# Optimization experiments

Measured on AMD Instinct MI355X. Metric: run time of the kernel, lower is better.

The kernel has to match this reference:

```python
import jax, jax.numpy as jnp
import numpy as np

K_SIGN = 100000.0   # tanh sharpness approximating sign()
EPS = 1e-05         # acos clamp epsilon


def setup_inputs() -> dict:
    key = jax.random.key(0)
    B, N, KV = 2, 8, 64
    contour = jax.random.uniform(key, (B, N, KV, 2), dtype=jnp.float32)  # values in [0,1]
    return {"contour": contour, "size": 128}


def reference(contour, size):
    b, n, kv, _ = contour.shape
    dt = contour.dtype
    # pixel grid, normalized by size (matches torch meshgrid 'ij' + reshape(-1,2)/size)
    g = jnp.arange(size, dtype=dt)
    mesh = jnp.stack(jnp.meshgrid(g, g, indexing="ij"), axis=-1).reshape(-1, 2) / size  # (S2, 2)

    c = contour.reshape(b * n, 1, kv, 2)          # (bn, 1, kv, 2)
    diff = c - mesh[None, :, None, :]             # (bn, S2, kv, 2)
    roll_diff = jnp.roll(diff, -1, axis=2)        # next vertex

    # sign = diff * swap(roll_diff); sign[...,1]-sign[...,0] = d_y*rd_x - d_x*rd_y
    cross = diff[..., 1] * roll_diff[..., 0] - diff[..., 0] * roll_diff[..., 1]
    sign = jnp.tanh(K_SIGN * cross)               # (bn, S2, kv)

    norm_diff = jnp.linalg.norm(diff, axis=3)
    norm_roll = jnp.linalg.norm(roll_diff, axis=3)
    scalar = jnp.sum(diff * roll_diff, axis=3)
    cosang = jnp.clip(scalar / (norm_diff * norm_roll), -1.0 + EPS, 1.0 - EPS)
    angles = jnp.arccos(cosang)                   # (bn, S2, kv)

    sum_angles = jnp.clip(jnp.abs(jnp.sum(sign * angles, axis=2) / (2.0 * jnp.pi)), 0.0, 1.0)
    return sum_angles.reshape(b, n, size, size)
```

## Files before the change

### kernel.cpp

```cpp
#include <hip/hip_runtime.h>
#include <math.h>

#define BLOCK 256
#define SPLIT 4
#define MAX_KV_LDS 1024

__device__ __forceinline__ float fast_tanh_k(float cross)
{
    float e = __expf(cross * 200000.0f);
    return fmaf(-2.0f, __builtin_amdgcn_rcpf(e + 1.0f), 1.0f);
}

__device__ __forceinline__ float fast_acos(float x)
{
    float y = fabsf(x);
    float p = fmaf(-0.0187293f, y, 0.0742610f);
    p = fmaf(p, y, -0.2121144f);
    p = fmaf(p, y, 1.5707288f);
    float a = sqrtf(1.0f - y) * p;
    return (x >= 0.0f) ? a : (3.14159265358979f - a);
}

template <typename VP>
__device__ __forceinline__ float winding_partial(VP vsrc, int kv, int k0, int k1,
                                                 float mx, float my)
{
    float acc = 0.0f;
    if (k0 >= k1) return acc;
    float2 v = vsrc[k0];
    float dx = v.x - mx, dy = v.y - my;
    float nd2 = fmaf(dx, dx, dy * dy);

    #pragma unroll 4
    for (int k = k0; k < k1; ++k) {
        int kn = k + 1;
        if (kn == kv) kn = 0;
        float2 vn = vsrc[kn];
        float rx = vn.x - mx, ry = vn.y - my;
        float cross = dy * rx - dx * ry;
        float dot   = fmaf(dx, rx, dy * ry);
        float nr2   = fmaf(rx, rx, ry * ry);
        float cosang = dot * __builtin_amdgcn_rsqf(nd2 * nr2);
        cosang = __builtin_amdgcn_fmed3f(cosang, -1.0f + 1e-5f, 1.0f - 1e-5f);
        acc = fmaf(fast_tanh_k(cross), fast_acos(cosang), acc);
        dx = rx; dy = ry; nd2 = nr2;
    }
    return acc;
}

__global__ __launch_bounds__(BLOCK)
void contour_mask_kernel(const float2* __restrict__ contour,
                         const int* __restrict__ size_ptr,
                         float* __restrict__ out,
                         int out_size, int in0_elems)
{
    __shared__ float2 verts[MAX_KV_LDS];

    const int size     = *size_ptr;
    const int S2       = size * size;
    const int bn_total = out_size / S2;
    const int kv       = in0_elems / (bn_total * 2);

    const int tid   = threadIdx.x;
    const int idx4  = blockIdx.x * BLOCK + tid;
    const int pixel = idx4 >> 2;
    const int seg   = tid & (SPLIT - 1);

    const int p_first = (blockIdx.x * BLOCK) >> 2;
    const int p_last  = ((blockIdx.x + 1) * BLOCK - 1) >> 2;
    const int bn0     = p_first / S2;
    const bool use_lds = (kv <= MAX_KV_LDS) && (bn0 == p_last / S2);

    if (use_lds) {
        for (int i = tid; i < kv; i += BLOCK)
            verts[i] = contour[(size_t)bn0 * kv + i];
    }
    __syncthreads();

    float acc = 0.0f;
    if (pixel < out_size) {
        const int bn = pixel / S2;
        const int p  = pixel - bn * S2;
        const float inv_size = 1.0f / (float)size;
        const int pi = p / size;
        const int pj = p - pi * size;
        const float mx = (float)pi * inv_size;
        const float my = (float)pj * inv_size;

        const int q  = (kv + SPLIT - 1) / SPLIT;
        const int k0 = seg * q;
        const int k1 = min(k0 + q, kv);

        if (use_lds)
            acc = winding_partial(verts, kv, k0, k1, mx, my);
        else
            acc = winding_partial(contour + (size_t)bn * kv, kv, k0, k1, mx, my);
    }

    acc += __shfl_xor(acc, 1, 64);
    acc += __shfl_xor(acc, 2, 64);

    if (pixel < out_size && seg == 0) {
        float res = fabsf(acc) * 0.15915494309189535f;
        out[pixel] = fminf(res, 1.0f);
    }
}

extern "C" void kernel_launch(void* const* d_in, const int* in_sizes, int n_in,
                              void* d_out, int out_size, void* d_ws, size_t ws_size,
                              hipStream_t stream)
{
    const float2* contour  = (const float2*)d_in[0];
    const int*    size_ptr = (const int*)d_in[1];
    float*        out      = (float*)d_out;

    const long long threads = (long long)out_size * SPLIT;
    const int blocks = (int)((threads + BLOCK - 1) / BLOCK);
    contour_mask_kernel<<<blocks, BLOCK, 0, stream>>>(
        contour, size_ptr, out, out_size, in_sizes[0]);
}
```

Measured before the change: 77.79 us.

## Process two pixels per thread with packed float2 vector math

Each thread now evaluates two adjacent pixels against the same vertex segment, using 2-wide vector types so the compiler can emit packed FP32 ops (v_pk_fma/mul). Each vertex value loaded from LDS is reused across both pixels, and the grid shrinks by half. Results are written as float2. Transcendentals stay scalar, so the gain is limited to the arithmetic and load portions, and halving the thread count may reduce latency hiding.

```diff
diff --git a/kernel.cpp b/kernel.cpp
--- a/kernel.cpp
+++ b/kernel.cpp
@@ -3,22 +3,58 @@
 
 #define BLOCK 256
 #define SPLIT 4
+#define PPT   2
 #define MAX_KV_LDS 1024
 
-__device__ __forceinline__ float fast_tanh_k(float cross)
+typedef float v2f __attribute__((ext_vector_type(2)));
+
+__device__ __forceinline__ float rsq1(float x)  { return __builtin_amdgcn_rsqf(x); }
+__device__ __forceinline__ float sqrt1(float x) { return __builtin_amdgcn_sqrtf(x); }
+__device__ __forceinline__ float rcp1(float x)  { return __builtin_amdgcn_rcpf(x); }
+
+template <typename VP>
+__device__ __forceinline__ v2f winding_partial_pk(VP vsrc, int kv, int k0, int k1,
+                                                  v2f mx2, v2f my2)
 {
-    float e = __expf(cross * 200000.0f);
-    return fmaf(-2.0f, __builtin_amdgcn_rcpf(e + 1.0f), 1.0f);
-}
+    v2f acc = {0.0f, 0.0f};
+    if (k0 >= k1) return acc;
+    float2 v = vsrc[k0];
+    v2f dx2 = v.x - mx2;
+    v2f dy2 = v.y - my2;
+    v2f nd2 = dx2 * dx2 + dy2 * dy2;
 
-__device__ __forceinline__ float fast_acos(float x)
-{
-    float y = fabsf(x);
-    float p = fmaf(-0.0187293f, y, 0.0742610f);
-    p = fmaf(p, y, -0.2121144f);
-    p = fmaf(p, y, 1.5707288f);
-    float a = sqrtf(1.0f - y) * p;
-    return (x >= 0.0f) ? a : (3.14159265358979f - a);
+    #pragma unroll 4
+    for (int k = k0; k < k1; ++k) {
+        int kn = k + 1;
+        if (kn == kv) kn = 0;
+        float2 vn = vsrc[kn];
+        v2f rx2 = vn.x - mx2;
+        v2f ry2 = vn.y - my2;
+        v2f cross = dy2 * rx2 - dx2 * ry2;
+        v2f dot   = dx2 * rx2 + dy2 * ry2;
+        v2f nr2   = rx2 * rx2 + ry2 * ry2;
+        v2f n2    = nd2 * nr2;
+        v2f inv   = { rsq1(n2.x), rsq1(n2.y) };
+        v2f c     = dot * inv;
+        c.x = __builtin_amdgcn_fmed3f(c.x, -0.99999f, 0.99999f);
+        c.y = __builtin_amdgcn_fmed3f(c.y, -0.99999f, 0.99999f);
+        v2f y = { fabsf(c.x), fabsf(c.y) };
+        v2f p = -0.0187293f * y + 0.0742610f;
+        p = p * y + -0.2121144f;
+        p = p * y + 1.5707288f;
+        v2f s = { sqrt1(1.0f - y.x), sqrt1(1.0f - y.y) };
+        v2f a = s * p;
+        v2f ar = 3.14159265358979f - a;
+        a.x = (c.x >= 0.0f) ? a.x : ar.x;
+        a.y = (c.y >= 0.0f) ? a.y : ar.y;
+        v2f t = cross * 200000.0f;
+        v2f th;
+        th.x = fmaf(-2.0f, rcp1(__expf(t.x) + 1.0f), 1.0f);
+        th.y = fmaf(-2.0f, rcp1(__expf(t.y) + 1.0f), 1.0f);
+        acc = acc + th * a;
+        dx2 = rx2; dy2 = ry2; nd2 = nr2;
+    }
+    return acc;
 }
 
 template <typename VP>
@@ -30,8 +66,6 @@
     float2 v = vsrc[k0];
     float dx = v.x - mx, dy = v.y - my;
     float nd2 = fmaf(dx, dx, dy * dy);
-
-    #pragma unroll 4
     for (int k = k0; k < k1; ++k) {
         int kn = k + 1;
         if (kn == kv) kn = 0;
@@ -40,9 +74,16 @@
         float cross = dy * rx - dx * ry;
         float dot   = fmaf(dx, rx, dy * ry);
         float nr2   = fmaf(rx, rx, ry * ry);
-        float cosang = dot * __builtin_amdgcn_rsqf(nd2 * nr2);
-        cosang = __builtin_amdgcn_fmed3f(cosang, -1.0f + 1e-5f, 1.0f - 1e-5f);
-        acc = fmaf(fast_tanh_k(cross), fast_acos(cosang), acc);
+        float c = dot * rsq1(nd2 * nr2);
+        c = __builtin_amdgcn_fmed3f(c, -0.99999f, 0.99999f);
+        float yy = fabsf(c);
+        float p = fmaf(-0.0187293f, yy, 0.0742610f);
+        p = fmaf(p, yy, -0.2121144f);
+        p = fmaf(p, yy, 1.5707288f);
+        float a = sqrt1(1.0f - yy) * p;
+        a = (c >= 0.0f) ? a : (3.14159265358979f - a);
+        float th = fmaf(-2.0f, rcp1(__expf(cross * 200000.0f) + 1.0f), 1.0f);
+        acc = fmaf(th, a, acc);
         dx = rx; dy = ry; nd2 = nr2;
     }
     return acc;
@@ -61,15 +102,15 @@
     const int bn_total = out_size / S2;
     const int kv       = in0_elems / (bn_total * 2);
 
-    const int tid   = threadIdx.x;
-    const int idx4  = blockIdx.x * BLOCK + tid;
-    const int pixel = idx4 >> 2;
-    const int seg   = tid & (SPLIT - 1);
+    const int tid  = threadIdx.x;
+    const int PIX_PER_BLOCK = (BLOCK / SPLIT) * PPT;
+    const int base = blockIdx.x * PIX_PER_BLOCK;
 
-    const int p_first = (blockIdx.x * BLOCK) >> 2;
-    const int p_last  = ((blockIdx.x + 1) * BLOCK - 1) >> 2;
-    const int bn0     = p_first / S2;
-    const bool use_lds = (kv <= MAX_KV_LDS) && (bn0 == p_last / S2);
+    const int bn0 = base / S2;
+    const int rem = base - bn0 * S2;
+    const bool one_image = (rem + PIX_PER_BLOCK <= S2) &&
+                           (base + PIX_PER_BLOCK <= out_size);
+    const bool use_lds = (kv <= MAX_KV_LDS) && one_image;
 
     if (use_lds) {
         for (int i = tid; i < kv; i += BLOCK)
@@ -77,32 +118,57 @@
     }
     __syncthreads();
 
-    float acc = 0.0f;
-    if (pixel < out_size) {
-        const int bn = pixel / S2;
-        const int p  = pixel - bn * S2;
-        const float inv_size = 1.0f / (float)size;
-        const int pi = p / size;
-        const int pj = p - pi * size;
-        const float mx = (float)pi * inv_size;
-        const float my = (float)pj * inv_size;
+    const int seg = tid & (SPLIT - 1);
+    const int q   = (kv + SPLIT - 1) / SPLIT;
+    const int k0  = min(seg * q, kv);
+    const int k1  = min(k0 + q, kv);
+    const float inv_size = 1.0f / (float)size;
+    const float INV2PI = 0.15915494309189535f;
 
-        const int q  = (kv + SPLIT - 1) / SPLIT;
-        const int k0 = seg * q;
-        const int k1 = min(k0 + q, kv);
+    if (use_lds) {
+        const int pi0 = rem / size;
+        const int pj0 = rem - pi0 * size;
+        const int t   = (tid / SPLIT) * PPT;
 
-        if (use_lds)
-            acc = winding_partial(verts, kv, k0, k1, mx, my);
-        else
-            acc = winding_partial(contour + (size_t)bn * kv, kv, k0, k1, mx, my);
-    }
+        int pjA = pj0 + t, piA = pi0;
+        while (pjA >= size) { pjA -= size; ++piA; }
+        int pjB = pjA + 1, piB = piA;
+        if (pjB >= size) { pjB = 0; ++piB; }
 
-    acc += __shfl_xor(acc, 1, 64);
-    acc += __shfl_xor(acc, 2, 64);
+        v2f mx2 = { piA * inv_size, piB * inv_size };
+        v2f my2 = { pjA * inv_size, pjB * inv_size };
 
-    if (pixel < out_size && seg == 0) {
-        float res = fabsf(acc) * 0.15915494309189535f;
-        out[pixel] = fminf(res, 1.0f);
+        v2f acc = winding_partial_pk(verts, kv, k0, k1, mx2, my2);
+        acc.x += __shfl_xor(acc.x, 1, 64);
+        acc.y += __shfl_xor(acc.y, 1, 64);
+        acc.x += __shfl_xor(acc.x, 2, 64);
+        acc.y += __shfl_xor(acc.y, 2, 64);
+
+        if (seg == 0) {
+            float2 res;
+            res.x = fminf(fabsf(acc.x) * INV2PI, 1.0f);
+            res.y = fminf(fabsf(acc.y) * INV2PI, 1.0f);
+            *(float2*)(out + base + t) = res;
+        }
+    } else {
+        #pragma unroll
+        for (int px = 0; px < PPT; ++px) {
+            const int pixel = base + (tid / SPLIT) * PPT + px;
+            float a = 0.0f;
+            int bn = 0;
+            if (pixel < out_size) {
+                bn = pixel / S2;
+                const int p  = pixel - bn * S2;
+                const int pi = p / size;
+                const int pj = p - pi * size;
+                a = winding_partial(contour + (size_t)bn * kv, kv, k0, k1,
+                                    pi * inv_size, pj * inv_size);
+            }
+            a += __shfl_xor(a, 1, 64);
+            a += __shfl_xor(a, 2, 64);
+            if (pixel < out_size && seg == 0)
+                out[pixel] = fminf(fabsf(a) * INV2PI, 1.0f);
+        }
     }
 }
 
@@ -114,8 +180,8 @@
     const int*    size_ptr = (const int*)d_in[1];
     float*        out      = (float*)d_out;
 
-    const long long threads = (long long)out_size * SPLIT;
-    const int blocks = (int)((threads + BLOCK - 1) / BLOCK);
+    const int PIX_PER_BLOCK = (BLOCK / SPLIT) * PPT;
+    const int blocks = (out_size + PIX_PER_BLOCK - 1) / PIX_PER_BLOCK;
     contour_mask_kernel<<<blocks, BLOCK, 0, stream>>>(
         contour, size_ptr, out, out_size, in_sizes[0]);
 }
```

After: 68.02 us. 1.14x faster.
